# Kernel optimization log

Hardware: AMD Instinct MI355X
Metric: run time of the kernel (lower is better)

Reference implementation:

```python
import math
import jax, jax.numpy as jnp
import numpy as np

B, T, D = 4, 2048, 768
NH, DH = 12, 64

def setup_inputs() -> dict:
    key = jax.random.key(0)
    k1, k2, k3 = jax.random.split(key, 3)
    scale_attn = 1.0 / math.sqrt(D)
    scale_proj = 1.0 / math.sqrt(D)
    return {
        "x": jax.random.normal(k1, (B, T, D), dtype=jnp.float32),
        "w_attn": jax.random.normal(k2, (D, 3 * D), dtype=jnp.float32) * scale_attn,
        "b_attn": jnp.zeros((3 * D,), dtype=jnp.float32),
        "w_proj": jax.random.normal(k3, (D, D), dtype=jnp.float32) * scale_proj,
        "b_proj": jnp.zeros((D,), dtype=jnp.float32),
    }

def reference(x, w_attn, b_attn, w_proj, b_proj):
    Bx, Tx, Dx = x.shape
    qkv = x @ w_attn + b_attn                     # [B, T, 3D]
    q, k, v = jnp.split(qkv, 3, axis=-1)          # each [B, T, D]
    # [B, T, D] -> [B, NH, T, DH]
    def to_heads(t):
        return t.reshape(Bx, Tx, NH, DH).transpose(0, 2, 1, 3)
    q, k, v = to_heads(q), to_heads(k), to_heads(v)
    attn = jnp.einsum("bhqd,bhkd->bhqk", q, k) / math.sqrt(DH)
    causal = jnp.tril(jnp.ones((Tx, Tx), dtype=bool))
    attn = jnp.where(causal[None, None, :, :], attn, -jnp.inf)
    attn = jax.nn.softmax(attn, axis=-1)
    out = jnp.einsum("bhqk,bhkd->bhqd", attn, v)  # [B, NH, T, DH]
    out = out.transpose(0, 2, 1, 3).reshape(Bx, Tx, Dx)
    out = out @ w_proj + b_proj
    return (out, (k, v))
```

## Files before the change

kernel.cpp:

```cpp
#include <hip/hip_runtime.h>
#include <hip/hip_bf16.h>

typedef unsigned short ushort_t;
typedef __attribute__((ext_vector_type(8))) short short8;
typedef __attribute__((ext_vector_type(4))) float f32x4;

#define B_    4
#define T_    2048
#define D_    768
#define NH_   12
#define DH_   64
#define KDIM  768

__device__ __forceinline__ ushort_t f2bf(float f) {
  union { float f; unsigned u; } c; c.f = f;
  unsigned u = c.u;
  return (ushort_t)((u + 0x7FFFu + ((u >> 16) & 1u)) >> 16);
}

__device__ __forceinline__ unsigned cvt_pk_bf16(float lo, float hi) {
  unsigned r;
  asm("v_cvt_pk_bf16_f32 %0, %1, %2" : "=v"(r) : "v"(lo), "v"(hi));
  return r;
}

__device__ __forceinline__ void gload_lds16(const void* g, void* l) {
  __builtin_amdgcn_global_load_lds(
      (const __attribute__((address_space(1))) unsigned int*)g,
      (__attribute__((address_space(3))) unsigned int*)l, 16, 0, 0);
}

__global__ void cvt_bf16_vec(const float* __restrict__ in,
                             ushort_t* __restrict__ out, int n4) {
  int i = blockIdx.x * blockDim.x + threadIdx.x;
  if (i >= n4) return;
  float4 v = ((const float4*)in)[i];
  ushort4 o;
  o.x = f2bf(v.x); o.y = f2bf(v.y); o.z = f2bf(v.z); o.w = f2bf(v.w);
  ((ushort4*)out)[i] = o;
}

__global__ void transpose_cvt(const float* __restrict__ in,
                              ushort_t* __restrict__ out, int R, int C) {
  __shared__ float tile[32][33];
  int c0 = blockIdx.x * 32, r0 = blockIdx.y * 32;
  int tx = threadIdx.x, ty = threadIdx.y;
#pragma unroll
  for (int j = 0; j < 32; j += 8)
    tile[ty + j][tx] = in[(size_t)(r0 + ty + j) * C + c0 + tx];
  __syncthreads();
#pragma unroll
  for (int j = 0; j < 32; j += 8)
    out[(size_t)(c0 + ty + j) * R + r0 + tx] = f2bf(tile[tx][ty + j]);
}

__device__ __forceinline__ void gemm128_mainloop(
    const ushort_t* __restrict__ A, const ushort_t* __restrict__ BT,
    int m0, int n0, ushort_t* lds, f32x4 acc[4][4]) {
  const int t = threadIdx.x;
  const int l = t & 63;
  const int w = t >> 6;
  const int wm = w >> 1, wn = w & 1;
  const int c0 = t, c1 = t + 256;
  const ushort_t* ga0 = A + (size_t)(m0 + (c0 >> 2)) * KDIM + ((c0 & 3) << 3);
  const ushort_t* ga1 = A + (size_t)(m0 + (c1 >> 2)) * KDIM + ((c1 & 3) << 3);
  const ushort_t* gb0 = BT + (size_t)(n0 + (c0 >> 2)) * KDIM + ((c0 & 3) << 3);
  const ushort_t* gb1 = BT + (size_t)(n0 + (c1 >> 2)) * KDIM + ((c1 & 3) << 3);
  ushort_t* la0 = lds + (0 * 256 + w * 64) * 8;
  ushort_t* la1 = lds + (1 * 256 + w * 64) * 8;
  ushort_t* lb0 = lds + 4096 + (0 * 256 + w * 64) * 8;
  ushort_t* lb1 = lds + 4096 + (1 * 256 + w * 64) * 8;
  const int frag_off = ((l & 15) * 32) + ((l >> 4) * 8);

  for (int k0 = 0; k0 < KDIM; k0 += 32) {
    gload_lds16(ga0 + k0, la0);
    gload_lds16(ga1 + k0, la1);
    gload_lds16(gb0 + k0, lb0);
    gload_lds16(gb1 + k0, lb1);
    __syncthreads();
    short8 af[4], bfv[4];
#pragma unroll
    for (int mt = 0; mt < 4; ++mt)
      af[mt] = *(const short8*)&lds[(wm * 64 + mt * 16) * 32 + frag_off];
#pragma unroll
    for (int nt = 0; nt < 4; ++nt)
      bfv[nt] = *(const short8*)&lds[4096 + (wn * 64 + nt * 16) * 32 + frag_off];
#pragma unroll
    for (int mt = 0; mt < 4; ++mt)
#pragma unroll
      for (int nt = 0; nt < 4; ++nt)
        acc[mt][nt] = __builtin_amdgcn_mfma_f32_16x16x32_bf16(
            af[mt], bfv[nt], acc[mt][nt], 0, 0, 0);
    __syncthreads();
  }
}

__global__ __launch_bounds__(256) void gemm_qkv_kernel(
    const ushort_t* __restrict__ xbf, const ushort_t* __restrict__ wT,
    const float* __restrict__ bias, ushort_t* __restrict__ qbf,
    float* __restrict__ kout, float* __restrict__ vout,
    ushort_t* __restrict__ kbf, ushort_t* __restrict__ vtbf) {
  __shared__ ushort_t lds[8192];
  int bid = blockIdx.x;
  int m0 = (bid & 63) << 7;
  int n0 = (bid >> 6) << 7;
  f32x4 acc[4][4];
  f32x4 zero = {0.f, 0.f, 0.f, 0.f};
#pragma unroll
  for (int a = 0; a < 4; ++a)
#pragma unroll
    for (int b = 0; b < 4; ++b) acc[a][b] = zero;
  gemm128_mainloop(xbf, wT, m0, n0, lds, acc);

  const float QSC = 0.125f * 1.44269504089f;
  const int l = threadIdx.x & 63, w = threadIdx.x >> 6;
  const int wm = w >> 1, wn = w & 1;
  const int sec = n0 / 768;
  const int b = m0 >> 11;
  const int tt_base = (m0 & 2047) + wm * 64;
#pragma unroll
  for (int nt = 0; nt < 4; ++nt) {
    int n = n0 + wn * 64 + nt * 16 + (l & 15);
    float bv = bias[n];
    int nn = n - sec * 768;
    int h = nn >> 6, dh = nn & 63;
    size_t head_base = ((size_t)(b * NH_ + h) * T_);
#pragma unroll
    for (int mt = 0; mt < 4; ++mt) {
      int tt0 = tt_base + mt * 16 + ((l >> 4) << 2);
      float vals[4];
#pragma unroll
      for (int r = 0; r < 4; ++r) vals[r] = acc[mt][nt][r] + bv;
      if (sec == 0) {
#pragma unroll
        for (int r = 0; r < 4; ++r)
          qbf[((head_base + tt0 + r) << 6) + dh] = f2bf(vals[r] * QSC);
      } else if (sec == 1) {
#pragma unroll
        for (int r = 0; r < 4; ++r) {
          size_t idx = ((head_base + tt0 + r) << 6) + dh;
          kout[idx] = vals[r];
          kbf[idx] = f2bf(vals[r]);
        }
      } else {
#pragma unroll
        for (int r = 0; r < 4; ++r)
          vout[((head_base + tt0 + r) << 6) + dh] = vals[r];
        ushort4 pk;
        pk.x = f2bf(vals[0]); pk.y = f2bf(vals[1]);
        pk.z = f2bf(vals[2]); pk.w = f2bf(vals[3]);
        *(ushort4*)&vtbf[((size_t)(b * NH_ + h) * DH_ + dh) * T_ + tt0] = pk;
      }
    }
  }
}

__global__ __launch_bounds__(256) void gemm_proj_kernel(
    const ushort_t* __restrict__ abf, const ushort_t* __restrict__ wT,
    const float* __restrict__ bias, float* __restrict__ out) {
  __shared__ ushort_t lds[8192];
  int bid = blockIdx.x;
  int m0 = (bid & 63) << 7;
  int n0 = (bid >> 6) << 7;
  f32x4 acc[4][4];
  f32x4 zero = {0.f, 0.f, 0.f, 0.f};
#pragma unroll
  for (int a = 0; a < 4; ++a)
#pragma unroll
    for (int b = 0; b < 4; ++b) acc[a][b] = zero;
  gemm128_mainloop(abf, wT, m0, n0, lds, acc);

  const int l = threadIdx.x & 63, w = threadIdx.x >> 6;
  const int wm = w >> 1, wn = w & 1;
#pragma unroll
  for (int nt = 0; nt < 4; ++nt) {
    int n = n0 + wn * 64 + nt * 16 + (l & 15);
    float bv = bias[n];
#pragma unroll
    for (int mt = 0; mt < 4; ++mt) {
#pragma unroll
      for (int r = 0; r < 4; ++r) {
        int m = m0 + wm * 64 + mt * 16 + ((l >> 4) << 2) + r;
        out[(size_t)m * D_ + n] = acc[mt][nt][r] + bv;
      }
    }
  }
}

__device__ __forceinline__ void strip_exp_store(
    f32x4 s4[4], int gq, bool diag, int kvb, int g, int qi, char* pbase) {
  if (diag) {
#pragma unroll
    for (int nt = 0; nt < 4; ++nt)
#pragma unroll
      for (int r = 0; r < 4; ++r) {
        int gk = kvb + nt * 16 + g * 4 + r;
        if (gk > gq) s4[nt][r] = -1e30f;
      }
  }
#pragma unroll
  for (int nt = 0; nt < 4; ++nt) {
    float p0 = exp2f(s4[nt][0]);
    float p1 = exp2f(s4[nt][1]);
    float p2 = exp2f(s4[nt][2]);
    float p3 = exp2f(s4[nt][3]);
    uint2 pk;
    pk.x = cvt_pk_bf16(p0, p1);
    pk.y = cvt_pk_bf16(p2, p3);
    *(uint2*)(pbase + ((nt * 32 + g * 8) ^ ((qi & 7) << 4))) = pk;
  }
}

__global__ __launch_bounds__(256, 3) void attn_fwd_kernel(
    const ushort_t* __restrict__ qbf, const ushort_t* __restrict__ kbf,
    const ushort_t* __restrict__ vtbf, ushort_t* __restrict__ obf) {
  __shared__ ushort_t Kl[3][4096];
  __shared__ ushort_t Vt[2][4096];
  __shared__ ushort_t Pl[4][1024];
  const int bid = blockIdx.x;
  const int swz = (bid & 7) * 96 + (bid >> 3);
  const int jp = swz & 15;
  const int bh = swz >> 4;
  const int qlo = jp << 6, qhi = (31 - jp) << 6;
  const int lastH = 31 - jp, lastL = jp;
  const int t = threadIdx.x, l = t & 63, w = t >> 6;
  const int g = l >> 4, qi = l & 15;

  const ushort_t* Qb = qbf + (size_t)bh * T_ * DH_;
  const ushort_t* Kb = kbf + (size_t)bh * T_ * DH_;
  const ushort_t* Vb = vtbf + (size_t)bh * DH_ * T_;

  const int row0 = t >> 3, ch0 = t & 7, row1 = row0 + 32;
  const ushort_t* gK0 = Kb + row0 * DH_ + ((ch0 ^ (row0 & 7)) << 3);
  const ushort_t* gK1 = Kb + row1 * DH_ + ((ch0 ^ (row1 & 7)) << 3);
  const ushort_t* gV0 = Vb + (size_t)row0 * T_ + ((ch0 ^ (row0 & 7)) << 3);
  const ushort_t* gV1 = Vb + (size_t)row1 * T_ + ((ch0 ^ (row1 & 7)) << 3);

  short8 aqH[2], aqL[2];
  {
    const int qrH = qhi + w * 16 + qi, qrL = qlo + w * 16 + qi;
    aqH[0] = *(const short8*)&Qb[(size_t)qrH * DH_ + (g << 3)];
    aqH[1] = *(const short8*)&Qb[(size_t)qrH * DH_ + (g << 3) + 32];
    aqL[0] = *(const short8*)&Qb[(size_t)qrL * DH_ + (g << 3)];
    aqL[1] = *(const short8*)&Qb[(size_t)qrL * DH_ + (g << 3) + 32];
  }

  short8 ones;
#pragma unroll
  for (int j = 0; j < 8; ++j) ones[j] = (short)0x3F80;

  f32x4 oH[4], oL[4], alH, alL;
  f32x4 zero = {0.f, 0.f, 0.f, 0.f};
#pragma unroll
  for (int nt = 0; nt < 4; ++nt) { oH[nt] = zero; oL[nt] = zero; }
  alH = zero; alL = zero;

  gload_lds16(gK0, &Kl[0][w * 512]);
  gload_lds16(gK1, &Kl[0][2048 + w * 512]);
  gload_lds16(gV0, &Vt[0][w * 512]);
  gload_lds16(gV1, &Vt[0][2048 + w * 512]);
  gload_lds16(gK0 + 4096, &Kl[1][w * 512]);
  gload_lds16(gK1 + 4096, &Kl[1][2048 + w * 512]);

  char* pb = (char*)&Pl[w][0] + qi * 128;
  int kb = 0;

  for (int kt = 0; kt <= lastH; ++kt) {
    const int kvb = kt << 6;
    const int vb = kt & 1;
    if (kt < lastH) {
      asm volatile("s_waitcnt vmcnt(2)" ::: "memory");
    } else {
      asm volatile("s_waitcnt vmcnt(0)" ::: "memory");
    }
    __builtin_amdgcn_sched_barrier(0);
    __builtin_amdgcn_s_barrier();
    __builtin_amdgcn_sched_barrier(0);
    if (kt + 1 <= lastH) {
      gload_lds16(gV0 + (size_t)(kt + 1) * 64, &Vt[vb ^ 1][w * 512]);
      gload_lds16(gV1 + (size_t)(kt + 1) * 64, &Vt[vb ^ 1][2048 + w * 512]);
    }
    if (kt + 2 <= lastH) {
      int kb2 = kb + 2 >= 3 ? kb - 1 : kb + 2;
      gload_lds16(gK0 + (size_t)(kt + 2) * 4096, &Kl[kb2][w * 512]);
      gload_lds16(gK1 + (size_t)(kt + 2) * 4096, &Kl[kb2][2048 + w * 512]);
    }
    const bool loAct = (kt <= lastL);

    f32x4 s4H[4], s4L[4];
#pragma unroll
    for (int nt = 0; nt < 4; ++nt) { s4H[nt] = zero; s4L[nt] = zero; }
#pragma unroll
    for (int h2 = 0; h2 < 2; ++h2) {
      short8 bk[4];
#pragma unroll
      for (int nt = 0; nt < 4; ++nt)
        bk[nt] = *(const short8*)&Kl[kb][((nt * 16 + qi) << 6) +
                                         (((g + 4 * h2) ^ (qi & 7)) << 3)];
#pragma unroll
      for (int nt = 0; nt < 4; ++nt)
        s4H[nt] = __builtin_amdgcn_mfma_f32_16x16x32_bf16(bk[nt], aqH[h2],
                                                          s4H[nt], 0, 0, 0);
      if (loAct) {
#pragma unroll
        for (int nt = 0; nt < 4; ++nt)
          s4L[nt] = __builtin_amdgcn_mfma_f32_16x16x32_bf16(bk[nt], aqL[h2],
                                                            s4L[nt], 0, 0, 0);
      }
    }

    strip_exp_store(s4H, qhi + w * 16 + qi, kt == lastH, kvb, g, qi, pb);
#pragma unroll
    for (int k2 = 0; k2 < 2; ++k2) {
      short8 av[4];
#pragma unroll
      for (int nt = 0; nt < 4; ++nt)
        av[nt] = *(const short8*)&Vt[vb][((nt * 16 + qi) << 6) +
                                         (((g + 4 * k2) ^ (qi & 7)) << 3)];
      short8 pf = *(const short8*)(pb + ((g * 16 + k2 * 64) ^ ((qi & 7) << 4)));
#pragma unroll
      for (int nt = 0; nt < 4; ++nt)
        oH[nt] = __builtin_amdgcn_mfma_f32_16x16x32_bf16(av[nt], pf, oH[nt],
                                                         0, 0, 0);
      alH = __builtin_amdgcn_mfma_f32_16x16x32_bf16(ones, pf, alH, 0, 0, 0);
    }

    if (loAct) {
      strip_exp_store(s4L, qlo + w * 16 + qi, kt == lastL, kvb, g, qi, pb);
#pragma unroll
      for (int k2 = 0; k2 < 2; ++k2) {
        short8 av[4];
#pragma unroll
        for (int nt = 0; nt < 4; ++nt)
          av[nt] = *(const short8*)&Vt[vb][((nt * 16 + qi) << 6) +
                                           (((g + 4 * k2) ^ (qi & 7)) << 3)];
        short8 pf = *(const short8*)(pb + ((g * 16 + k2 * 64) ^ ((qi & 7) << 4)));
#pragma unroll
        for (int nt = 0; nt < 4; ++nt)
          oL[nt] = __builtin_amdgcn_mfma_f32_16x16x32_bf16(av[nt], pf, oL[nt],
                                                           0, 0, 0);
        alL = __builtin_amdgcn_mfma_f32_16x16x32_bf16(ones, pf, alL, 0, 0, 0);
      }
    }
    kb = kb + 1 >= 3 ? 0 : kb + 1;
  }

  const int b = bh / NH_, h = bh - b * NH_;
#pragma unroll
  for (int s = 0; s < 2; ++s) {
    f32x4* o = s ? oL : oH;
    float inv = 1.f / (s ? alL[0] : alH[0]);
    int qs = (s ? qlo : qhi) + w * 16 + qi;
    size_t rowb = (size_t)(b * T_ + qs) * D_ + h * DH_;
#pragma unroll
    for (int nt = 0; nt < 4; ++nt) {
      ushort4 pk;
      pk.x = f2bf(o[nt][0] * inv);
      pk.y = f2bf(o[nt][1] * inv);
      pk.z = f2bf(o[nt][2] * inv);
      pk.w = f2bf(o[nt][3] * inv);
      *(ushort4*)&obf[rowb + nt * 16 + g * 4] = pk;
    }
  }
}

extern "C" void kernel_launch(void* const* d_in, const int* in_sizes, int n_in,
                              void* d_out, int out_size, void* d_ws, size_t ws_size,
                              hipStream_t stream) {
  const float* x      = (const float*)d_in[0];
  const float* w_attn = (const float*)d_in[1];
  const float* b_attn = (const float*)d_in[2];
  const float* w_proj = (const float*)d_in[3];
  const float* b_proj = (const float*)d_in[4];

  float* out  = (float*)d_out;
  float* kout = out + (size_t)B_ * T_ * D_;
  float* vout = kout + (size_t)B_ * T_ * D_;

  char* ws = (char*)d_ws;
  ushort_t* xbf = (ushort_t*)(ws);
  ushort_t* wTa = (ushort_t*)(ws + 12582912);
  ushort_t* wTp = (ushort_t*)(ws + 16121856);
  ushort_t* qbf = (ushort_t*)(ws + 17301504);
  ushort_t* kbf = (ushort_t*)(ws + 29884416);
  ushort_t* vtbf = (ushort_t*)(ws + 42467328);
  ushort_t* abf = xbf;

  cvt_bf16_vec<<<6144, 256, 0, stream>>>(x, xbf, (B_ * T_ * D_) / 4);
  dim3 tb(32, 8);
  transpose_cvt<<<dim3(72, 24), tb, 0, stream>>>(w_attn, wTa, D_, 3 * D_);
  transpose_cvt<<<dim3(24, 24), tb, 0, stream>>>(w_proj, wTp, D_, D_);

  gemm_qkv_kernel<<<64 * 18, 256, 0, stream>>>(xbf, wTa, b_attn, qbf, kout, vout,
                                               kbf, vtbf);
  attn_fwd_kernel<<<48 * 16, 256, 0, stream>>>(qbf, kbf, vtbf, abf);
  gemm_proj_kernel<<<64 * 6, 256, 0, stream>>>(abf, wTp, b_proj, out);
}
```

Baseline: 143.1 us.

## Keep softmax probabilities in registers via permuted K rows, dropping P LDS staging

```diff
diff --git a/kernel.cpp b/kernel.cpp
--- a/kernel.cpp
+++ b/kernel.cpp
@@ -187,36 +187,38 @@
   }
 }
 
-__device__ __forceinline__ void strip_exp_store(
-    f32x4 s4[4], int gq, bool diag, int kvb, int g, int qi, char* pbase) {
+__device__ __forceinline__ void strip_make_w(
+    f32x4 s4[4], int gq, bool diag, int kvb, int g, short8 w[2]) {
   if (diag) {
 #pragma unroll
-    for (int nt = 0; nt < 4; ++nt)
-#pragma unroll
-      for (int r = 0; r < 4; ++r) {
-        int gk = kvb + nt * 16 + g * 4 + r;
-        if (gk > gq) s4[nt][r] = -1e30f;
-      }
-  }
-#pragma unroll
-  for (int nt = 0; nt < 4; ++nt) {
-    float p0 = exp2f(s4[nt][0]);
-    float p1 = exp2f(s4[nt][1]);
-    float p2 = exp2f(s4[nt][2]);
-    float p3 = exp2f(s4[nt][3]);
-    uint2 pk;
-    pk.x = cvt_pk_bf16(p0, p1);
-    pk.y = cvt_pk_bf16(p2, p3);
-    *(uint2*)(pbase + ((nt * 32 + g * 8) ^ ((qi & 7) << 4))) = pk;
-  }
-}
-
-__global__ __launch_bounds__(256, 3) void attn_fwd_kernel(
+    for (int nt = 0; nt < 4; ++nt) {
+      int kb0 = kvb + ((nt >> 1) << 5) + (g << 3) + ((nt & 1) << 2);
+#pragma unroll
+      for (int r = 0; r < 4; ++r)
+        if (kb0 + r > gq) s4[nt][r] = -1e30f;
+    }
+  }
+  float p[4][4];
+#pragma unroll
+  for (int nt = 0; nt < 4; ++nt)
+#pragma unroll
+    for (int r = 0; r < 4; ++r) p[nt][r] = exp2f(s4[nt][r]);
+#pragma unroll
+  for (int k2 = 0; k2 < 2; ++k2) {
+    union { unsigned u[4]; short8 s; } c;
+    c.u[0] = cvt_pk_bf16(p[2 * k2][0], p[2 * k2][1]);
+    c.u[1] = cvt_pk_bf16(p[2 * k2][2], p[2 * k2][3]);
+    c.u[2] = cvt_pk_bf16(p[2 * k2 + 1][0], p[2 * k2 + 1][1]);
+    c.u[3] = cvt_pk_bf16(p[2 * k2 + 1][2], p[2 * k2 + 1][3]);
+    w[k2] = c.s;
+  }
+}
+
+__global__ __launch_bounds__(256, 4) void attn_fwd_kernel(
     const ushort_t* __restrict__ qbf, const ushort_t* __restrict__ kbf,
     const ushort_t* __restrict__ vtbf, ushort_t* __restrict__ obf) {
   __shared__ ushort_t Kl[3][4096];
   __shared__ ushort_t Vt[2][4096];
-  __shared__ ushort_t Pl[4][1024];
   const int bid = blockIdx.x;
   const int swz = (bid & 7) * 96 + (bid >> 3);
   const int jp = swz & 15;
@@ -231,10 +233,12 @@
   const ushort_t* Vb = vtbf + (size_t)bh * DH_ * T_;
 
   const int row0 = t >> 3, ch0 = t & 7, row1 = row0 + 32;
-  const ushort_t* gK0 = Kb + row0 * DH_ + ((ch0 ^ (row0 & 7)) << 3);
-  const ushort_t* gK1 = Kb + row1 * DH_ + ((ch0 ^ (row1 & 7)) << 3);
-  const ushort_t* gV0 = Vb + (size_t)row0 * T_ + ((ch0 ^ (row0 & 7)) << 3);
-  const ushort_t* gV1 = Vb + (size_t)row1 * T_ + ((ch0 ^ (row1 & 7)) << 3);
+  const int sw0 = (row0 & 3) | (((row0 >> 3) & 1) << 2);
+  const int sw1 = (row1 & 3) | (((row1 >> 3) & 1) << 2);
+  const ushort_t* gK0 = Kb + row0 * DH_ + ((ch0 ^ sw0) << 3);
+  const ushort_t* gK1 = Kb + row1 * DH_ + ((ch0 ^ sw1) << 3);
+  const ushort_t* gV0 = Vb + (size_t)row0 * T_ + ((ch0 ^ sw0) << 3);
+  const ushort_t* gV1 = Vb + (size_t)row1 * T_ + ((ch0 ^ sw1) << 3);
 
   short8 aqH[2], aqL[2];
   {
@@ -255,6 +259,9 @@
   for (int nt = 0; nt < 4; ++nt) { oH[nt] = zero; oL[nt] = zero; }
   alH = zero; alL = zero;
 
+  const int swzq = (qi & 3) | (((qi >> 2) & 1) << 2);
+  const int swzv = (qi & 3) | (((qi >> 3) & 1) << 2);
+
   gload_lds16(gK0, &Kl[0][w * 512]);
   gload_lds16(gK1, &Kl[0][2048 + w * 512]);
   gload_lds16(gV0, &Vt[0][w * 512]);
@@ -262,7 +269,6 @@
   gload_lds16(gK0 + 4096, &Kl[1][w * 512]);
   gload_lds16(gK1 + 4096, &Kl[1][2048 + w * 512]);
 
-  char* pb = (char*)&Pl[w][0] + qi * 128;
   int kb = 0;
 
   for (int kt = 0; kt <= lastH; ++kt) {
@@ -292,11 +298,13 @@
     for (int nt = 0; nt < 4; ++nt) { s4H[nt] = zero; s4L[nt] = zero; }
 #pragma unroll
     for (int h2 = 0; h2 < 2; ++h2) {
+      const int slotk = ((g + 4 * h2) ^ swzq) << 3;
       short8 bk[4];
 #pragma unroll
-      for (int nt = 0; nt < 4; ++nt)
-        bk[nt] = *(const short8*)&Kl[kb][((nt * 16 + qi) << 6) +
-                                         (((g + 4 * h2) ^ (qi & 7)) << 3)];
+      for (int nt = 0; nt < 4; ++nt) {
+        int row = ((nt >> 1) << 5) + ((qi >> 2) << 3) + ((nt & 1) << 2) + (qi & 3);
+        bk[nt] = *(const short8*)&Kl[kb][(row << 6) + slotk];
+      }
 #pragma unroll
       for (int nt = 0; nt < 4; ++nt)
         s4H[nt] = __builtin_amdgcn_mfma_f32_16x16x32_bf16(bk[nt], aqH[h2],
@@ -309,37 +317,29 @@
       }
     }
 
-    strip_exp_store(s4H, qhi + w * 16 + qi, kt == lastH, kvb, g, qi, pb);
+    short8 wH[2], wL[2];
+    strip_make_w(s4H, qhi + w * 16 + qi, kt == lastH, kvb, g, wH);
+    if (loAct)
+      strip_make_w(s4L, qlo + w * 16 + qi, kt == lastL, kvb, g, wL);
+
 #pragma unroll
     for (int k2 = 0; k2 < 2; ++k2) {
+      const int slotv = ((g + 4 * k2) ^ swzv) << 3;
       short8 av[4];
 #pragma unroll
       for (int nt = 0; nt < 4; ++nt)
-        av[nt] = *(const short8*)&Vt[vb][((nt * 16 + qi) << 6) +
-                                         (((g + 4 * k2) ^ (qi & 7)) << 3)];
-      short8 pf = *(const short8*)(pb + ((g * 16 + k2 * 64) ^ ((qi & 7) << 4)));
+        av[nt] = *(const short8*)&Vt[vb][((nt * 16 + qi) << 6) + slotv];
 #pragma unroll
       for (int nt = 0; nt < 4; ++nt)
-        oH[nt] = __builtin_amdgcn_mfma_f32_16x16x32_bf16(av[nt], pf, oH[nt],
+        oH[nt] = __builtin_amdgcn_mfma_f32_16x16x32_bf16(av[nt], wH[k2], oH[nt],
                                                          0, 0, 0);
-      alH = __builtin_amdgcn_mfma_f32_16x16x32_bf16(ones, pf, alH, 0, 0, 0);
-    }
-
-    if (loAct) {
-      strip_exp_store(s4L, qlo + w * 16 + qi, kt == lastL, kvb, g, qi, pb);
-#pragma unroll
-      for (int k2 = 0; k2 < 2; ++k2) {
-        short8 av[4];
+      alH = __builtin_amdgcn_mfma_f32_16x16x32_bf16(ones, wH[k2], alH, 0, 0, 0);
+      if (loAct) {
 #pragma unroll
         for (int nt = 0; nt < 4; ++nt)
-          av[nt] = *(const short8*)&Vt[vb][((nt * 16 + qi) << 6) +
-                                           (((g + 4 * k2) ^ (qi & 7)) << 3)];
-        short8 pf = *(const short8*)(pb + ((g * 16 + k2 * 64) ^ ((qi & 7) << 4)));
-#pragma unroll
-        for (int nt = 0; nt < 4; ++nt)
-          oL[nt] = __builtin_amdgcn_mfma_f32_16x16x32_bf16(av[nt], pf, oL[nt],
-                                                           0, 0, 0);
-        alL = __builtin_amdgcn_mfma_f32_16x16x32_bf16(ones, pf, alL, 0, 0, 0);
+          oL[nt] = __builtin_amdgcn_mfma_f32_16x16x32_bf16(av[nt], wL[k2],
+                                                           oL[nt], 0, 0, 0);
+        alL = __builtin_amdgcn_mfma_f32_16x16x32_bf16(ones, wL[k2], alL, 0, 0, 0);
       }
     }
     kb = kb + 1 >= 3 ? 0 : kb + 1;
```

New measurement: 160.2 us. +11.9%, slower.
